# Performance work log

Hardware: AMD Instinct MI355X
Metric: run time of the kernel (lower is better)

## Reference

```python
import jax, jax.numpy as jnp
import numpy as np

LOSS_WEIGHT = 1.0
INTENSITY_WEIGHT = 0.5


def setup_inputs() -> dict:
    key = jax.random.key(0)
    k1, k2 = jax.random.split(key)
    N = 8192
    adv_pc = jax.random.normal(k1, (N, 4), dtype=jnp.float32)
    ori_pc = jax.random.normal(k2, (N, 4), dtype=jnp.float32)
    return {"adv_pc": adv_pc, "ori_pc": ori_pc}


def reference(adv_pc, ori_pc):
    # Scale the intensity channel (index 3) by intensity_weight, as in forward().
    scale = jnp.array([1.0, 1.0, 1.0, INTENSITY_WEIGHT], dtype=adv_pc.dtype)
    a = adv_pc * scale  # [N, 4]
    b = ori_pc * scale  # [M, 4]
    # knn_points with K=1 returns SQUARED euclidean distance to nearest neighbor.
    # Use the ||a||^2 + ||b||^2 - 2 a.b expansion to avoid an [N, M, 4] diff tensor.
    a2 = jnp.sum(a * a, axis=-1)          # [N]
    b2 = jnp.sum(b * b, axis=-1)          # [M]
    cross = jnp.einsum('nd,md->nm', a, b)  # [N, M]
    sqdist = a2[:, None] + b2[None, :] - 2.0 * cross  # [N, M]
    min_d = jnp.min(sqdist, axis=-1)      # per-adv-point nearest sq distance, [N]
    hd = jnp.max(min_d)                   # one-sided Hausdorff (squared)
    # original keeps the batch dim of size 1 after max(-1)
    return jnp.reshape(hd * LOSS_WEIGHT, (1,))
```

## Files before the change

### kernel.cpp

```cpp
#include <hip/hip_runtime.h>
#include <math.h>

#define TILE 512

__global__ __launch_bounds__(256) void hd_partial_min(
    const float* __restrict__ adv, const float* __restrict__ ori,
    float* __restrict__ ws, float* __restrict__ out,
    int N, int M, int N_pad, int chunks)
{
    __shared__ float4 sb[TILE];
    __shared__ float  sb2[TILE];

    const int tid = threadIdx.x;
    const int i   = blockIdx.x * 256 + tid;

    if (blockIdx.x == 0 && blockIdx.y == 0 && tid == 0) out[0] = 0.0f;

    float4 a = make_float4(0.f, 0.f, 0.f, 0.f);
    if (i < N) {
        a = ((const float4*)adv)[i];
        a.w *= 0.5f;
    }

    float m0 = INFINITY, m1 = INFINITY, m2 = INFINITY, m3 = INFINITY;

    for (int base = blockIdx.y * TILE; base < M; base += chunks * TILE) {
        for (int k = tid; k < TILE; k += 256) {
            int j = base + k;
            float4 b = make_float4(0.f, 0.f, 0.f, 0.f);
            float b2 = INFINITY;
            if (j < M) {
                b = ((const float4*)ori)[j];
                b.w *= 0.5f;
                b2 = b.x*b.x + b.y*b.y + b.z*b.z + b.w*b.w;
            }
            sb[k]  = b;
            sb2[k] = b2;
        }
        __syncthreads();

        for (int j = 0; j < TILE; j += 4) {
            float4 p0 = sb[j+0], p1 = sb[j+1], p2 = sb[j+2], p3 = sb[j+3];
            float  q0 = sb2[j+0], q1 = sb2[j+1], q2 = sb2[j+2], q3 = sb2[j+3];
            float c0 = fmaf(a.x, p0.x, fmaf(a.y, p0.y, fmaf(a.z, p0.z, a.w * p0.w)));
            float c1 = fmaf(a.x, p1.x, fmaf(a.y, p1.y, fmaf(a.z, p1.z, a.w * p1.w)));
            float c2 = fmaf(a.x, p2.x, fmaf(a.y, p2.y, fmaf(a.z, p2.z, a.w * p2.w)));
            float c3 = fmaf(a.x, p3.x, fmaf(a.y, p3.y, fmaf(a.z, p3.z, a.w * p3.w)));
            m0 = fminf(m0, fmaf(-2.f, c0, q0));
            m1 = fminf(m1, fmaf(-2.f, c1, q1));
            m2 = fminf(m2, fmaf(-2.f, c2, q2));
            m3 = fminf(m3, fmaf(-2.f, c3, q3));
        }
        __syncthreads();
    }

    if (i < N) {
        float a2 = a.x*a.x + a.y*a.y + a.z*a.z + a.w*a.w;
        float d  = a2 + fminf(fminf(m0, m1), fminf(m2, m3));
        ws[(size_t)blockIdx.y * N_pad + i] = fmaxf(d, 0.0f);
    }
}

__global__ __launch_bounds__(256) void hd_reduce(
    const float* __restrict__ ws, float* __restrict__ out,
    int N, int N_pad, int rows)
{
    int i = blockIdx.x * 256 + threadIdx.x;
    float m = 0.0f;
    if (i < N) {
        m = INFINITY;
        for (int r = 0; r < rows; ++r)
            m = fminf(m, ws[(size_t)r * N_pad + i]);
    }
    for (int off = 32; off >= 1; off >>= 1)
        m = fmaxf(m, __shfl_down(m, off, 64));
    __shared__ float smax[4];
    int lane = threadIdx.x & 63, wave = threadIdx.x >> 6;
    if (lane == 0) smax[wave] = m;
    __syncthreads();
    if (threadIdx.x == 0) {
        float bm = fmaxf(fmaxf(smax[0], smax[1]), fmaxf(smax[2], smax[3]));
        atomicMax((unsigned int*)out, __float_as_uint(bm));
    }
}

extern "C" void kernel_launch(void* const* d_in, const int* in_sizes, int n_in,
                              void* d_out, int out_size, void* d_ws, size_t ws_size,
                              hipStream_t stream) {
    const float* adv = (const float*)d_in[0];
    const float* ori = (const float*)d_in[1];
    float* out = (float*)d_out;
    float* ws  = (float*)d_ws;

    int N = in_sizes[0] / 4;
    int M = in_sizes[1] / 4;

    int nblk_x = (N + 255) / 256;
    int N_pad  = nblk_x * 256;

    int chunks = 16;
    while (chunks > 1 && (size_t)chunks * (size_t)N_pad * sizeof(float) > ws_size)
        chunks >>= 1;
    int ntiles = (M + TILE - 1) / TILE;
    if (chunks > ntiles) chunks = ntiles;
    if (chunks < 1) chunks = 1;

    hd_partial_min<<<dim3(nblk_x, chunks), 256, 0, stream>>>(
        adv, ori, ws, out, N, M, N_pad, chunks);
    hd_reduce<<<nblk_x, 256, 0, stream>>>(ws, out, N, N_pad, chunks);
}
```

Baseline: 73.69 us.

## Register-block 8 adv points per thread and fold -2 scale into adv coords

Each thread now holds 8 adv points in registers and reuses every LDS-loaded ori point across all of them. This cuts shared-memory reads per FMA. The -2 factor and the intensity weight are folded into the adv coordinates ahead of time, so each distance costs four FMAs with b2 as the accumulator. The tile shrinks to 64 and chunks grow to up to 128 to keep enough blocks in flight, which raises workspace traffic and the reduce loop length. The reduce kernel is unrolled by four.

Measured after the change: 76.13 us. 1.03x slower.

```diff
diff --git a/kernel.cpp b/kernel.cpp
--- a/kernel.cpp
+++ b/kernel.cpp
@@ -1,9 +1,11 @@
 #include <hip/hip_runtime.h>
 #include <math.h>
 
-#define TILE 512
+#define THREADS 256
+#define APT 8
+#define TILE 64
 
-__global__ __launch_bounds__(256) void hd_partial_min(
+__global__ __launch_bounds__(THREADS) void hd_partial_min(
     const float* __restrict__ adv, const float* __restrict__ ori,
     float* __restrict__ ws, float* __restrict__ out,
     int N, int M, int N_pad, int chunks)
@@ -12,20 +14,28 @@
     __shared__ float  sb2[TILE];
 
     const int tid = threadIdx.x;
-    const int i   = blockIdx.x * 256 + tid;
-
     if (blockIdx.x == 0 && blockIdx.y == 0 && tid == 0) out[0] = 0.0f;
 
-    float4 a = make_float4(0.f, 0.f, 0.f, 0.f);
-    if (i < N) {
-        a = ((const float4*)adv)[i];
-        a.w *= 0.5f;
+    const int base_i = blockIdx.x * (THREADS * APT) + tid;
+
+    float4 a[APT];
+    #pragma unroll
+    for (int k = 0; k < APT; ++k) {
+        int i = base_i + k * THREADS;
+        float4 v = make_float4(0.f, 0.f, 0.f, 0.f);
+        if (i < N) v = ((const float4*)adv)[i];
+        a[k].x = -2.0f * v.x;
+        a[k].y = -2.0f * v.y;
+        a[k].z = -2.0f * v.z;
+        a[k].w = -v.w;
     }
 
-    float m0 = INFINITY, m1 = INFINITY, m2 = INFINITY, m3 = INFINITY;
+    float m[APT];
+    #pragma unroll
+    for (int k = 0; k < APT; ++k) m[k] = INFINITY;
 
     for (int base = blockIdx.y * TILE; base < M; base += chunks * TILE) {
-        for (int k = tid; k < TILE; k += 256) {
+        for (int k = tid; k < TILE; k += THREADS) {
             int j = base + k;
             float4 b = make_float4(0.f, 0.f, 0.f, 0.f);
             float b2 = INFINITY;
@@ -41,45 +51,60 @@
 
         for (int j = 0; j < TILE; j += 4) {
             float4 p0 = sb[j+0], p1 = sb[j+1], p2 = sb[j+2], p3 = sb[j+3];
-            float  q0 = sb2[j+0], q1 = sb2[j+1], q2 = sb2[j+2], q3 = sb2[j+3];
-            float c0 = fmaf(a.x, p0.x, fmaf(a.y, p0.y, fmaf(a.z, p0.z, a.w * p0.w)));
-            float c1 = fmaf(a.x, p1.x, fmaf(a.y, p1.y, fmaf(a.z, p1.z, a.w * p1.w)));
-            float c2 = fmaf(a.x, p2.x, fmaf(a.y, p2.y, fmaf(a.z, p2.z, a.w * p2.w)));
-            float c3 = fmaf(a.x, p3.x, fmaf(a.y, p3.y, fmaf(a.z, p3.z, a.w * p3.w)));
-            m0 = fminf(m0, fmaf(-2.f, c0, q0));
-            m1 = fminf(m1, fmaf(-2.f, c1, q1));
-            m2 = fminf(m2, fmaf(-2.f, c2, q2));
-            m3 = fminf(m3, fmaf(-2.f, c3, q3));
+            float4 q  = ((const float4*)sb2)[j >> 2];
+            #pragma unroll
+            for (int k = 0; k < APT; ++k) {
+                float ax = a[k].x, ay = a[k].y, az = a[k].z, aw = a[k].w;
+                float d0 = fmaf(ax, p0.x, fmaf(ay, p0.y, fmaf(az, p0.z, fmaf(aw, p0.w, q.x))));
+                float d1 = fmaf(ax, p1.x, fmaf(ay, p1.y, fmaf(az, p1.z, fmaf(aw, p1.w, q.y))));
+                float d2 = fmaf(ax, p2.x, fmaf(ay, p2.y, fmaf(az, p2.z, fmaf(aw, p2.w, q.z))));
+                float d3 = fmaf(ax, p3.x, fmaf(ay, p3.y, fmaf(az, p3.z, fmaf(aw, p3.w, q.w))));
+                m[k] = fminf(fminf(m[k], d0), fminf(d1, fminf(d2, d3)));
+            }
         }
         __syncthreads();
     }
 
-    if (i < N) {
-        float a2 = a.x*a.x + a.y*a.y + a.z*a.z + a.w*a.w;
-        float d  = a2 + fminf(fminf(m0, m1), fminf(m2, m3));
-        ws[(size_t)blockIdx.y * N_pad + i] = fmaxf(d, 0.0f);
+    #pragma unroll
+    for (int k = 0; k < APT; ++k) {
+        int i = base_i + k * THREADS;
+        if (i < N) {
+            float aa = a[k].x*a[k].x + a[k].y*a[k].y + a[k].z*a[k].z + a[k].w*a[k].w;
+            float d  = fmaf(0.25f, aa, m[k]);
+            ws[(size_t)blockIdx.y * N_pad + i] = fmaxf(d, 0.0f);
+        }
     }
 }
 
-__global__ __launch_bounds__(256) void hd_reduce(
+__global__ __launch_bounds__(THREADS) void hd_reduce(
     const float* __restrict__ ws, float* __restrict__ out,
     int N, int N_pad, int rows)
 {
-    int i = blockIdx.x * 256 + threadIdx.x;
+    int i = blockIdx.x * THREADS + threadIdx.x;
     float m = 0.0f;
     if (i < N) {
-        m = INFINITY;
-        for (int r = 0; r < rows; ++r)
-            m = fminf(m, ws[(size_t)r * N_pad + i]);
+        float m0 = INFINITY, m1 = INFINITY, m2 = INFINITY, m3 = INFINITY;
+        int r = 0;
+        for (; r + 3 < rows; r += 4) {
+            m0 = fminf(m0, ws[(size_t)(r+0) * N_pad + i]);
+            m1 = fminf(m1, ws[(size_t)(r+1) * N_pad + i]);
+            m2 = fminf(m2, ws[(size_t)(r+2) * N_pad + i]);
+            m3 = fminf(m3, ws[(size_t)(r+3) * N_pad + i]);
+        }
+        for (; r < rows; ++r)
+            m0 = fminf(m0, ws[(size_t)r * N_pad + i]);
+        m = fminf(fminf(m0, m1), fminf(m2, m3));
     }
     for (int off = 32; off >= 1; off >>= 1)
         m = fmaxf(m, __shfl_down(m, off, 64));
-    __shared__ float smax[4];
+    __shared__ float smax[THREADS / 64];
     int lane = threadIdx.x & 63, wave = threadIdx.x >> 6;
     if (lane == 0) smax[wave] = m;
     __syncthreads();
     if (threadIdx.x == 0) {
-        float bm = fmaxf(fmaxf(smax[0], smax[1]), fmaxf(smax[2], smax[3]));
+        float bm = smax[0];
+        #pragma unroll
+        for (int w = 1; w < THREADS / 64; ++w) bm = fmaxf(bm, smax[w]);
         atomicMax((unsigned int*)out, __float_as_uint(bm));
     }
 }
@@ -95,17 +120,16 @@
     int N = in_sizes[0] / 4;
     int M = in_sizes[1] / 4;
 
-    int nblk_x = (N + 255) / 256;
-    int N_pad  = nblk_x * 256;
+    int gx    = (N + THREADS * APT - 1) / (THREADS * APT);
+    int N_pad = gx * THREADS * APT;
 
-    int chunks = 16;
+    int chunks = (M + TILE - 1) / TILE;
+    if (chunks > 128) chunks = 128;
     while (chunks > 1 && (size_t)chunks * (size_t)N_pad * sizeof(float) > ws_size)
         chunks >>= 1;
-    int ntiles = (M + TILE - 1) / TILE;
-    if (chunks > ntiles) chunks = ntiles;
-    if (chunks < 1) chunks = 1;
 
-    hd_partial_min<<<dim3(nblk_x, chunks), 256, 0, stream>>>(
+    hd_partial_min<<<dim3(gx, chunks), THREADS, 0, stream>>>(
         adv, ori, ws, out, N, M, N_pad, chunks);
-    hd_reduce<<<nblk_x, 256, 0, stream>>>(ws, out, N, N_pad, chunks);
+    hd_reduce<<<(N + THREADS - 1) / THREADS, THREADS, 0, stream>>>(
+        ws, out, N, N_pad, chunks);
 }
```
